# Performance work log

Hardware: AMD Instinct MI355X
Metric: run time of the kernel (lower is better)

## Reference

```python
import jax, jax.numpy as jnp
import numpy as np

B, T, IN, H, FC, OUT = 512, 1024, 64, 128, 128, 1


def _glorot(key, shape, fan):
    bound = 1.0 / np.sqrt(fan)
    return jax.random.uniform(key, shape, jnp.float32, -bound, bound)


def setup_inputs() -> dict:
    key = jax.random.key(0)
    ks = jax.random.split(key, 16)
    inp = {"x": jax.random.normal(ks[0], (B, T, IN), jnp.float32)}
    # GRU layer 0 (input IN -> H), layer 1 (H -> H). PyTorch layout: [3H, in], [3H, H]
    inp["W_ih0"] = _glorot(ks[1], (3 * H, IN), H)
    inp["W_hh0"] = _glorot(ks[2], (3 * H, H), H)
    inp["b_ih0"] = _glorot(ks[3], (3 * H,), H)
    inp["b_hh0"] = _glorot(ks[4], (3 * H,), H)
    inp["W_ih1"] = _glorot(ks[5], (3 * H, H), H)
    inp["W_hh1"] = _glorot(ks[6], (3 * H, H), H)
    inp["b_ih1"] = _glorot(ks[7], (3 * H,), H)
    inp["b_hh1"] = _glorot(ks[8], (3 * H,), H)
    inp["fc1_w"] = _glorot(ks[9], (FC, H), H)
    inp["fc1_b"] = _glorot(ks[10], (FC,), H)
    inp["fc2_w"] = _glorot(ks[11], (OUT, FC), FC)
    inp["fc2_b"] = _glorot(ks[12], (OUT,), FC)
    return inp


def _gru_layer(x_seq, W_ih, W_hh, b_ih, b_hh):
    # x_seq: [T, B, in]. Precompute all input projections in one big GEMM.
    xg = jnp.einsum("tbi,gi->tbg", x_seq, W_ih) + b_ih  # [T, B, 3H]
    h0 = jnp.zeros((x_seq.shape[1], W_hh.shape[1]), x_seq.dtype)

    def step(h, xg_t):
        hg = h @ W_hh.T + b_hh  # [B, 3H]
        xr, xz, xn = jnp.split(xg_t, 3, axis=-1)
        hr, hz, hn = jnp.split(hg, 3, axis=-1)
        r = jax.nn.sigmoid(xr + hr)
        z = jax.nn.sigmoid(xz + hz)
        n = jnp.tanh(xn + r * hn)
        h_new = (1.0 - z) * n + z * h
        return h_new, h_new

    _, hs = jax.lax.scan(step, h0, xg)
    return hs  # [T, B, H]


def reference(x, W_ih0, W_hh0, b_ih0, b_hh0, W_ih1, W_hh1, b_ih1, b_hh1,
              fc1_w, fc1_b, fc2_w, fc2_b):
    xs = jnp.transpose(x, (1, 0, 2))  # [T, B, IN]
    h1 = _gru_layer(xs, W_ih0, W_hh0, b_ih0, b_hh0)  # dropout inactive (eval)
    h2 = _gru_layer(h1, W_ih1, W_hh1, b_ih1, b_hh1)
    last = h2[-1]  # [B, H] == gru_out[:, -1, :]
    y = jax.nn.relu(last @ fc1_w.T + fc1_b)
    return y @ fc2_w.T + fc2_b  # [B, OUT]
```

## Files before the change

### kernel.cpp

```cpp
#include <hip/hip_runtime.h>
#include <hip/hip_fp16.h>
#include <stdint.h>

#define BB   512
#define TT   1024
#define NIN  64
#define HH   128
#define GG   384
#define RPB  2
#define NWG  (BB / RPB)
#define NTHR (2 * GG)

typedef _Float16 half2v __attribute__((ext_vector_type(2)));

__device__ __forceinline__ float fdot2(uint32_t a, uint32_t b, float c) {
    return __builtin_amdgcn_fdot2(__builtin_bit_cast(half2v, a),
                                  __builtin_bit_cast(half2v, b), c, false);
}
__device__ __forceinline__ uint32_t pack2(float a, float b) {
    half2v v; v[0] = (_Float16)a; v[1] = (_Float16)b;
    return __builtin_bit_cast(uint32_t, v);
}
__device__ __forceinline__ uint4 pack8(const float* p) {
    uint4 r;
    r.x = pack2(p[0], p[1]); r.y = pack2(p[2], p[3]);
    r.z = pack2(p[4], p[5]); r.w = pack2(p[6], p[7]);
    return r;
}
__device__ __forceinline__ float sigm(float xv)     { return 1.f / (1.f + __expf(-xv)); }
__device__ __forceinline__ float tanhfast(float xv) { return 2.f / (1.f + __expf(-2.f * xv)) - 1.f; }

#define R8(M)  M(0) M(1) M(2) M(3) M(4) M(5) M(6) M(7)
#define R16(M) M(0) M(1) M(2) M(3) M(4) M(5) M(6) M(7) \
               M(8) M(9) M(10) M(11) M(12) M(13) M(14) M(15)
#define D4(A_, W_, S_) A_ = fdot2(W_.x, S_.x, A_); A_ = fdot2(W_.y, S_.y, A_); \
                       A_ = fdot2(W_.z, S_.z, A_); A_ = fdot2(W_.w, S_.w, A_);

__global__ __launch_bounds__(NTHR, 3) void gru_fused(
    const float* __restrict__ x,
    const float* __restrict__ Wih0, const float* __restrict__ Whh0,
    const float* __restrict__ bih0, const float* __restrict__ bhh0,
    const float* __restrict__ Wih1, const float* __restrict__ Whh1,
    const float* __restrict__ bih1, const float* __restrict__ bhh1,
    const float* __restrict__ fc1w, const float* __restrict__ fc1b,
    const float* __restrict__ fc2w, const float* __restrict__ fc2b,
    float* __restrict__ out)
{
    __shared__ __align__(16) uint32_t xh[RPB][NIN / 2];
    __shared__ __align__(16) uint32_t h0h[RPB][HH / 2];
    __shared__ __align__(16) uint32_t h1h[RPB][HH / 2];
    __shared__ float h0f[RPB][HH];
    __shared__ float h1f[RPB][HH];
    __shared__ float pX0[RPB][GG], pH0[RPB][GG];
    __shared__ float pX1[RPB][GG], pH1[RPB][GG];

    const int lid  = threadIdx.x;
    const int row0 = blockIdx.x * RPB;
    const bool is0 = (lid < GG);

#define DECLW(i) uint4 A##i; uint4 B##i;
    R16(DECLW)
    float bx, bh;

    if (is0) {
        const int g = lid;
        const float* wh = Whh0 + g * HH;
        const float* wi = Wih0 + g * NIN;
#define LA0(i) A##i = pack8(wh + 8 * (i));
#define LB0(i) B##i = pack8(wi + 8 * (i));
        R16(LA0)
        R8(LB0)
        bx = bih0[g]; bh = bhh0[g];
    } else {
        const int g = lid - GG;
        const float* wh = Whh1 + g * HH;
        const float* wi = Wih1 + g * HH;
        R16(LA0)
        R16(LB0)
        bx = bih1[g]; bh = bhh1[g];
    }

    if (lid < 2 * HH) {
        int r = lid >> 7, j = lid & (HH - 1);
        h0f[r][j] = 0.f; h1f[r][j] = 0.f;
    } else if (lid < 2 * HH + 2 * (HH / 2)) {
        int k2 = lid - 2 * HH;
        int r = k2 >> 6, c = k2 & 63;
        h0h[r][c] = 0u; h1h[r][c] = 0u;
    }

    float xreg = 0.f;
    if (lid >= GG + 2 * HH) {
        int j2 = lid - (GG + 2 * HH);
        int r = j2 >> 6, k = j2 & 63;
        const float* xp = x + (size_t)(row0 + r) * TT * NIN + k;
        ((__half*)&xh[r][0])[k] = __float2half(xp[0]);
        xreg = xp[NIN];
    }
    __syncthreads();

    const uint4* xh0v  = (const uint4*)&xh[0][0];
    const uint4* xh1v  = (const uint4*)&xh[1][0];
    const uint4* h0h0v = (const uint4*)&h0h[0][0];
    const uint4* h0h1v = (const uint4*)&h0h[1][0];
    const uint4* h1h0v = (const uint4*)&h1h[0][0];
    const uint4* h1h1v = (const uint4*)&h1h[1][0];

    for (int i = 0; i <= TT; ++i) {
        if (is0) {
            if (i < TT) {
                float ax0 = bx, ax1 = bx, ah0 = bh, ah1 = bh;
#define DX0(i) { uint4 s0 = xh0v[i], s1 = xh1v[i]; D4(ax0, B##i, s0) D4(ax1, B##i, s1) }
                R8(DX0)
#define DH0(i) { uint4 s0 = h0h0v[i], s1 = h0h1v[i]; D4(ah0, A##i, s0) D4(ah1, A##i, s1) }
                R16(DH0)
                pX0[0][lid] = ax0; pX0[1][lid] = ax1;
                pH0[0][lid] = ah0; pH0[1][lid] = ah1;
            }
        } else {
            if (i >= 1) {
                const int g = lid - GG;
                float ax0 = bx, ax1 = bx, ah0 = bh, ah1 = bh;
#define DL1(i) { uint4 p0 = h0h0v[i], p1 = h0h1v[i], q0 = h1h0v[i], q1 = h1h1v[i]; \
                 D4(ax0, B##i, p0) D4(ax1, B##i, p1) D4(ah0, A##i, q0) D4(ah1, A##i, q1) }
                R16(DL1)
                pX1[0][g] = ax0; pX1[1][g] = ax1;
                pH1[0][g] = ah0; pH1[1][g] = ah1;
            }
        }
        __syncthreads();

        if (lid < 2 * HH) {
            if (i < TT) {
                int r = lid >> 7, j = lid & (HH - 1);
                float sr = pX0[r][j]          + pH0[r][j];
                float sz = pX0[r][HH + j]     + pH0[r][HH + j];
                float xn = pX0[r][2 * HH + j];
                float hn = pH0[r][2 * HH + j];
                float rg = sigm(sr);
                float zg = sigm(sz);
                float ng = tanhfast(fmaf(rg, hn, xn));
                float hnew = fmaf(zg, h0f[r][j] - ng, ng);
                h0f[r][j] = hnew;
                ((__half*)&h0h[r][0])[j] = __float2half(hnew);
            }
        } else if (lid >= GG && lid < GG + 2 * HH) {
            if (i >= 1) {
                int t2 = lid - GG;
                int r = t2 >> 7, j = t2 & (HH - 1);
                float sr = pX1[r][j]          + pH1[r][j];
                float sz = pX1[r][HH + j]     + pH1[r][HH + j];
                float xn = pX1[r][2 * HH + j];
                float hn = pH1[r][2 * HH + j];
                float rg = sigm(sr);
                float zg = sigm(sz);
                float ng = tanhfast(fmaf(rg, hn, xn));
                float hnew = fmaf(zg, h1f[r][j] - ng, ng);
                h1f[r][j] = hnew;
                ((__half*)&h1h[r][0])[j] = __float2half(hnew);
            }
        } else if (lid >= GG + 2 * HH) {
            int j2 = lid - (GG + 2 * HH);
            int r = j2 >> 6, k = j2 & 63;
            if (i + 1 < TT) ((__half*)&xh[r][0])[k] = __float2half(xreg);
            if (i + 2 < TT) {
                const float* xp = x + (size_t)(row0 + r) * TT * NIN + (size_t)(i + 2) * NIN + k;
                xreg = xp[0];
            }
        }
        __syncthreads();
    }

    float yv = 0.f;
    if (lid < 2 * HH) {
        int r = lid >> 7, j = lid & (HH - 1);
        const float* fr = fc1w + j * HH;
        float acc = fc1b[j];
        #pragma unroll 8
        for (int k = 0; k < HH; ++k) acc = fmaf(fr[k], h1f[r][k], acc);
        yv = fmaxf(acc, 0.f) * fc2w[j];
        #pragma unroll
        for (int m = 1; m < 64; m <<= 1) yv += __shfl_xor(yv, m, 64);
    }
    __syncthreads();
    if (lid < 2 * HH && (lid & 63) == 0) pX0[0][lid >> 6] = yv;
    __syncthreads();
    if (lid < RPB) out[row0 + lid] = pX0[0][2 * lid] + pX0[0][2 * lid + 1] + fc2b[0];
}

extern "C" void kernel_launch(void* const* d_in, const int* in_sizes, int n_in,
                              void* d_out, int out_size, void* d_ws, size_t ws_size,
                              hipStream_t stream) {
    const float* x    = (const float*)d_in[0];
    const float* Wih0 = (const float*)d_in[1];
    const float* Whh0 = (const float*)d_in[2];
    const float* bih0 = (const float*)d_in[3];
    const float* bhh0 = (const float*)d_in[4];
    const float* Wih1 = (const float*)d_in[5];
    const float* Whh1 = (const float*)d_in[6];
    const float* bih1 = (const float*)d_in[7];
    const float* bhh1 = (const float*)d_in[8];
    const float* fc1w = (const float*)d_in[9];
    const float* fc1b = (const float*)d_in[10];
    const float* fc2w = (const float*)d_in[11];
    const float* fc2b = (const float*)d_in[12];

    gru_fused<<<dim3(NWG), dim3(NTHR), 0, stream>>>(
        x, Wih0, Whh0, bih0, bhh0, Wih1, Whh1, bih1, bhh1,
        fc1w, fc1b, fc2w, fc2b, (float*)d_out);
}
```

Baseline: 2.216 ms.

## Repartition GRU matvec work across thread groups with split-K and multi-gate outputs

Reassigns the 768 threads so each computes several gate outputs (3 or 4) over half the reduction dimension, rather than one gate output over the full dimension. Partial sums go to double-width shared buffers and are added in the gate-update phase. Shared-memory reads of the hidden state now feed more FMAs each, and the layer-1 input and recurrent projections run on separate thread groups. The x staging buffer is double-buffered and loaded as float2. The cost is extra shared-memory partial-sum traffic and additions, plus possible divergence across the more finely split roles.

```diff
diff --git a/kernel.cpp b/kernel.cpp
--- a/kernel.cpp
+++ b/kernel.cpp
@@ -2,14 +2,14 @@
 #include <hip/hip_fp16.h>
 #include <stdint.h>
 
-#define BB   512
 #define TT   1024
 #define NIN  64
 #define HH   128
 #define GG   384
 #define RPB  2
-#define NWG  (BB / RPB)
-#define NTHR (2 * GG)
+#define NWG  256
+#define NTHR 768
+
 
 typedef _Float16 half2v __attribute__((ext_vector_type(2)));
 
@@ -17,24 +17,29 @@
     return __builtin_amdgcn_fdot2(__builtin_bit_cast(half2v, a),
                                   __builtin_bit_cast(half2v, b), c, false);
 }
-__device__ __forceinline__ uint32_t pack2(float a, float b) {
+__device__ __forceinline__ uint32_t pack2f(float a, float b) {
     half2v v; v[0] = (_Float16)a; v[1] = (_Float16)b;
     return __builtin_bit_cast(uint32_t, v);
 }
 __device__ __forceinline__ uint4 pack8(const float* p) {
     uint4 r;
-    r.x = pack2(p[0], p[1]); r.y = pack2(p[2], p[3]);
-    r.z = pack2(p[4], p[5]); r.w = pack2(p[6], p[7]);
+    r.x = pack2f(p[0], p[1]); r.y = pack2f(p[2], p[3]);
+    r.z = pack2f(p[4], p[5]); r.w = pack2f(p[6], p[7]);
     return r;
 }
-__device__ __forceinline__ float sigm(float xv)     { return 1.f / (1.f + __expf(-xv)); }
-__device__ __forceinline__ float tanhfast(float xv) { return 2.f / (1.f + __expf(-2.f * xv)) - 1.f; }
-
-#define R8(M)  M(0) M(1) M(2) M(3) M(4) M(5) M(6) M(7)
-#define R16(M) M(0) M(1) M(2) M(3) M(4) M(5) M(6) M(7) \
-               M(8) M(9) M(10) M(11) M(12) M(13) M(14) M(15)
+__device__ __forceinline__ float sigm(float v)     { return 1.f / (1.f + __expf(-v)); }
+__device__ __forceinline__ float tanhfast(float v) { return 2.f / (1.f + __expf(-2.f * v)) - 1.f; }
+
 #define D4(A_, W_, S_) A_ = fdot2(W_.x, S_.x, A_); A_ = fdot2(W_.y, S_.y, A_); \
                        A_ = fdot2(W_.z, S_.z, A_); A_ = fdot2(W_.w, S_.w, A_);
+
+#define PK8(M_, g_) M_(g_,0) M_(g_,1) M_(g_,2) M_(g_,3) M_(g_,4) M_(g_,5) M_(g_,6) M_(g_,7)
+#define R8X(M_)     M_(0) M_(1) M_(2) M_(3) M_(4) M_(5) M_(6) M_(7)
+#define DWDEF(g_,k_) uint4 W##g_##_##k_;
+#define LW(g_,k_)    W##g_##_##k_ = pack8(wp + (g_)*ws + (k_)*8);
+#define DG(g_,k_) D4(a##g_##_0, W##g_##_##k_, s0_) D4(a##g_##_1, W##g_##_##k_, s1_)
+#define SK4(k_) { uint4 s0_ = pb0[k_], s1_ = pb1[k_]; DG(0,k_) DG(1,k_) DG(2,k_) DG(3,k_) }
+#define SK3(k_) { uint4 s0_ = pb0[k_], s1_ = pb1[k_]; DG(0,k_) DG(1,k_) DG(2,k_) }
 
 __global__ __launch_bounds__(NTHR, 3) void gru_fused(
     const float* __restrict__ x,
@@ -46,134 +51,155 @@
     const float* __restrict__ fc2w, const float* __restrict__ fc2b,
     float* __restrict__ out)
 {
-    __shared__ __align__(16) uint32_t xh[RPB][NIN / 2];
+    __shared__ __align__(16) uint32_t xh[2][RPB][NIN / 2];
     __shared__ __align__(16) uint32_t h0h[RPB][HH / 2];
     __shared__ __align__(16) uint32_t h1h[RPB][HH / 2];
     __shared__ float h0f[RPB][HH];
     __shared__ float h1f[RPB][HH];
-    __shared__ float pX0[RPB][GG], pH0[RPB][GG];
-    __shared__ float pX1[RPB][GG], pH1[RPB][GG];
+    __shared__ float pX0[RPB][GG];
+    __shared__ float pH0h[2][RPB][GG];
+    __shared__ float pX1h[2][RPB][GG];
+    __shared__ float pH1h[2][RPB][GG];
 
     const int lid  = threadIdx.x;
     const int row0 = blockIdx.x * RPB;
-    const bool is0 = (lid < GG);
-
-#define DECLW(i) uint4 A##i; uint4 B##i;
-    R16(DECLW)
-    float bx, bh;
-
-    if (is0) {
-        const int g = lid;
-        const float* wh = Whh0 + g * HH;
-        const float* wi = Wih0 + g * NIN;
-#define LA0(i) A##i = pack8(wh + 8 * (i));
-#define LB0(i) B##i = pack8(wi + 8 * (i));
-        R16(LA0)
-        R8(LB0)
-        bx = bih0[g]; bh = bhh0[g];
+
+    PK8(DWDEF,0) PK8(DWDEF,1) PK8(DWDEF,2) PK8(DWDEF,3)
+    float b0 = 0.f, b1 = 0.f, b2 = 0.f, b3 = 0.f;
+    int gq_ = 0, kh_ = 0;
+    const uint4 *pbA0 = nullptr, *pbA1 = nullptr;
+    float2 xr2 = {0.f, 0.f};
+
+    if (lid < 128) {
+        const int t = lid;
+        const float* wp = Wih0 + (3 * t) * NIN; const int ws = NIN;
+        PK8(LW,0) PK8(LW,1) PK8(LW,2)
+        b0 = bih0[3 * t]; b1 = bih0[3 * t + 1]; b2 = bih0[3 * t + 2];
+    } else if (lid < 320) {
+        const int t = lid - 128; gq_ = t >> 1; kh_ = t & 1;
+        const float* wp = Whh0 + (4 * gq_) * HH + kh_ * 64; const int ws = HH;
+        PK8(LW,0) PK8(LW,1) PK8(LW,2) PK8(LW,3)
+        if (!kh_) { b0 = bhh0[4*gq_]; b1 = bhh0[4*gq_+1]; b2 = bhh0[4*gq_+2]; b3 = bhh0[4*gq_+3]; }
+        pbA0 = (const uint4*)&h0h[0][0] + kh_ * 8;
+        pbA1 = (const uint4*)&h0h[1][0] + kh_ * 8;
+    } else if (lid < 512) {
+        const int t = lid - 320; gq_ = t >> 1; kh_ = t & 1;
+        const float* wp = Wih1 + (4 * gq_) * HH + kh_ * 64; const int ws = HH;
+        PK8(LW,0) PK8(LW,1) PK8(LW,2) PK8(LW,3)
+        if (!kh_) { b0 = bih1[4*gq_]; b1 = bih1[4*gq_+1]; b2 = bih1[4*gq_+2]; b3 = bih1[4*gq_+3]; }
+        pbA0 = (const uint4*)&h0h[0][0] + kh_ * 8;
+        pbA1 = (const uint4*)&h0h[1][0] + kh_ * 8;
+    } else if (lid < 704) {
+        const int t = lid - 512; gq_ = t >> 1; kh_ = t & 1;
+        const float* wp = Whh1 + (4 * gq_) * HH + kh_ * 64; const int ws = HH;
+        PK8(LW,0) PK8(LW,1) PK8(LW,2) PK8(LW,3)
+        if (!kh_) { b0 = bhh1[4*gq_]; b1 = bhh1[4*gq_+1]; b2 = bhh1[4*gq_+2]; b3 = bhh1[4*gq_+3]; }
+        pbA0 = (const uint4*)&h1h[0][0] + kh_ * 8;
+        pbA1 = (const uint4*)&h1h[1][0] + kh_ * 8;
     } else {
-        const int g = lid - GG;
-        const float* wh = Whh1 + g * HH;
-        const float* wi = Wih1 + g * HH;
-        R16(LA0)
-        R16(LB0)
-        bx = bih1[g]; bh = bhh1[g];
-    }
-
-    if (lid < 2 * HH) {
-        int r = lid >> 7, j = lid & (HH - 1);
+        const int idx = lid - 704, r = idx >> 5, c = idx & 31;
+        const float* xp = x + (size_t)(row0 + r) * TT * NIN + 2 * c;
+        xh[0][r][c] = pack2f(xp[0], xp[1]);
+        xr2 = *(const float2*)(xp + NIN);
+    }
+
+    if (lid < 128) {
+        int r = lid >> 6, c = lid & 63;
+        h0h[r][c] = 0u; h1h[r][c] = 0u;
+    }
+    if (lid < 256) {
+        int r = lid >> 7, j = lid & 127;
         h0f[r][j] = 0.f; h1f[r][j] = 0.f;
-    } else if (lid < 2 * HH + 2 * (HH / 2)) {
-        int k2 = lid - 2 * HH;
-        int r = k2 >> 6, c = k2 & 63;
-        h0h[r][c] = 0u; h1h[r][c] = 0u;
-    }
-
-    float xreg = 0.f;
-    if (lid >= GG + 2 * HH) {
-        int j2 = lid - (GG + 2 * HH);
-        int r = j2 >> 6, k = j2 & 63;
-        const float* xp = x + (size_t)(row0 + r) * TT * NIN + k;
-        ((__half*)&xh[r][0])[k] = __float2half(xp[0]);
-        xreg = xp[NIN];
     }
     __syncthreads();
 
-    const uint4* xh0v  = (const uint4*)&xh[0][0];
-    const uint4* xh1v  = (const uint4*)&xh[1][0];
-    const uint4* h0h0v = (const uint4*)&h0h[0][0];
-    const uint4* h0h1v = (const uint4*)&h0h[1][0];
-    const uint4* h1h0v = (const uint4*)&h1h[0][0];
-    const uint4* h1h1v = (const uint4*)&h1h[1][0];
-
     for (int i = 0; i <= TT; ++i) {
-        if (is0) {
+        if (lid < 128) {
             if (i < TT) {
-                float ax0 = bx, ax1 = bx, ah0 = bh, ah1 = bh;
-#define DX0(i) { uint4 s0 = xh0v[i], s1 = xh1v[i]; D4(ax0, B##i, s0) D4(ax1, B##i, s1) }
-                R8(DX0)
-#define DH0(i) { uint4 s0 = h0h0v[i], s1 = h0h1v[i]; D4(ah0, A##i, s0) D4(ah1, A##i, s1) }
-                R16(DH0)
-                pX0[0][lid] = ax0; pX0[1][lid] = ax1;
-                pH0[0][lid] = ah0; pH0[1][lid] = ah1;
+                const uint4* pb0 = (const uint4*)&xh[i & 1][0][0];
+                const uint4* pb1 = (const uint4*)&xh[i & 1][1][0];
+                float a0_0 = b0, a0_1 = b0, a1_0 = b1, a1_1 = b1, a2_0 = b2, a2_1 = b2;
+                R8X(SK3)
+                const int g0 = 3 * lid;
+                pX0[0][g0] = a0_0; pX0[0][g0+1] = a1_0; pX0[0][g0+2] = a2_0;
+                pX0[1][g0] = a0_1; pX0[1][g0+1] = a1_1; pX0[1][g0+2] = a2_1;
+            }
+        } else if (lid < 320) {
+            if (i < TT) {
+                const uint4 *pb0 = pbA0, *pb1 = pbA1;
+                float a0_0=b0,a0_1=b0,a1_0=b1,a1_1=b1,a2_0=b2,a2_1=b2,a3_0=b3,a3_1=b3;
+                R8X(SK4)
+                float4 v0 = {a0_0, a1_0, a2_0, a3_0};
+                float4 v1 = {a0_1, a1_1, a2_1, a3_1};
+                *(float4*)&pH0h[kh_][0][4 * gq_] = v0;
+                *(float4*)&pH0h[kh_][1][4 * gq_] = v1;
+            }
+        } else if (lid < 512) {
+            if (i >= 1) {
+                const uint4 *pb0 = pbA0, *pb1 = pbA1;
+                float a0_0=b0,a0_1=b0,a1_0=b1,a1_1=b1,a2_0=b2,a2_1=b2,a3_0=b3,a3_1=b3;
+                R8X(SK4)
+                float4 v0 = {a0_0, a1_0, a2_0, a3_0};
+                float4 v1 = {a0_1, a1_1, a2_1, a3_1};
+                *(float4*)&pX1h[kh_][0][4 * gq_] = v0;
+                *(float4*)&pX1h[kh_][1][4 * gq_] = v1;
+            }
+        } else if (lid < 704) {
+            if (i >= 1) {
+                const uint4 *pb0 = pbA0, *pb1 = pbA1;
+                float a0_0=b0,a0_1=b0,a1_0=b1,a1_1=b1,a2_0=b2,a2_1=b2,a3_0=b3,a3_1=b3;
+                R8X(SK4)
+                float4 v0 = {a0_0, a1_0, a2_0, a3_0};
+                float4 v1 = {a0_1, a1_1, a2_1, a3_1};
+                *(float4*)&pH1h[kh_][0][4 * gq_] = v0;
+                *(float4*)&pH1h[kh_][1][4 * gq_] = v1;
             }
         } else {
-            if (i >= 1) {
-                const int g = lid - GG;
-                float ax0 = bx, ax1 = bx, ah0 = bh, ah1 = bh;
-#define DL1(i) { uint4 p0 = h0h0v[i], p1 = h0h1v[i], q0 = h1h0v[i], q1 = h1h1v[i]; \
-                 D4(ax0, B##i, p0) D4(ax1, B##i, p1) D4(ah0, A##i, q0) D4(ah1, A##i, q1) }
-                R16(DL1)
-                pX1[0][g] = ax0; pX1[1][g] = ax1;
-                pH1[0][g] = ah0; pH1[1][g] = ah1;
-            }
+            const int idx = lid - 704, r = idx >> 5, c = idx & 31;
+            if (i + 1 < TT) xh[(i + 1) & 1][r][c] = pack2f(xr2.x, xr2.y);
+            if (i + 2 < TT)
+                xr2 = *(const float2*)(x + (size_t)(row0 + r) * TT * NIN
+                                         + (size_t)(i + 2) * NIN + 2 * c);
         }
         __syncthreads();
 
-        if (lid < 2 * HH) {
+        if (lid < 256) {
             if (i < TT) {
-                int r = lid >> 7, j = lid & (HH - 1);
-                float sr = pX0[r][j]          + pH0[r][j];
-                float sz = pX0[r][HH + j]     + pH0[r][HH + j];
-                float xn = pX0[r][2 * HH + j];
-                float hn = pH0[r][2 * HH + j];
-                float rg = sigm(sr);
-                float zg = sigm(sz);
-                float ng = tanhfast(fmaf(rg, hn, xn));
+                const int r = lid >> 7, j = lid & 127;
+                float xr_ = pX0[r][j], xz_ = pX0[r][HH + j], xn_ = pX0[r][2*HH + j];
+                float hr_ = pH0h[0][r][j]        + pH0h[1][r][j];
+                float hz_ = pH0h[0][r][HH + j]   + pH0h[1][r][HH + j];
+                float hn_ = pH0h[0][r][2*HH + j] + pH0h[1][r][2*HH + j];
+                float rg = sigm(xr_ + hr_);
+                float zg = sigm(xz_ + hz_);
+                float ng = tanhfast(fmaf(rg, hn_, xn_));
                 float hnew = fmaf(zg, h0f[r][j] - ng, ng);
                 h0f[r][j] = hnew;
                 ((__half*)&h0h[r][0])[j] = __float2half(hnew);
             }
-        } else if (lid >= GG && lid < GG + 2 * HH) {
+        } else if (lid < 512) {
             if (i >= 1) {
-                int t2 = lid - GG;
-                int r = t2 >> 7, j = t2 & (HH - 1);
-                float sr = pX1[r][j]          + pH1[r][j];
-                float sz = pX1[r][HH + j]     + pH1[r][HH + j];
-                float xn = pX1[r][2 * HH + j];
-                float hn = pH1[r][2 * HH + j];
-                float rg = sigm(sr);
-                float zg = sigm(sz);
-                float ng = tanhfast(fmaf(rg, hn, xn));
+                const int t = lid - 256, r = t >> 7, j = t & 127;
+                float xr_ = pX1h[0][r][j]        + pX1h[1][r][j];
+                float xz_ = pX1h[0][r][HH + j]   + pX1h[1][r][HH + j];
+                float xn_ = pX1h[0][r][2*HH + j] + pX1h[1][r][2*HH + j];
+                float hr_ = pH1h[0][r][j]        + pH1h[1][r][j];
+                float hz_ = pH1h[0][r][HH + j]   + pH1h[1][r][HH + j];
+                float hn_ = pH1h[0][r][2*HH + j] + pH1h[1][r][2*HH + j];
+                float rg = sigm(xr_ + hr_);
+                float zg = sigm(xz_ + hz_);
+                float ng = tanhfast(fmaf(rg, hn_, xn_));
                 float hnew = fmaf(zg, h1f[r][j] - ng, ng);
                 h1f[r][j] = hnew;
                 ((__half*)&h1h[r][0])[j] = __float2half(hnew);
             }
-        } else if (lid >= GG + 2 * HH) {
-            int j2 = lid - (GG + 2 * HH);
-            int r = j2 >> 6, k = j2 & 63;
-            if (i + 1 < TT) ((__half*)&xh[r][0])[k] = __float2half(xreg);
-            if (i + 2 < TT) {
-                const float* xp = x + (size_t)(row0 + r) * TT * NIN + (size_t)(i + 2) * NIN + k;
-                xreg = xp[0];
-            }
         }
         __syncthreads();
     }
 
     float yv = 0.f;
-    if (lid < 2 * HH) {
-        int r = lid >> 7, j = lid & (HH - 1);
+    if (lid < 256) {
+        const int r = lid >> 7, j = lid & 127;
         const float* fr = fc1w + j * HH;
         float acc = fc1b[j];
         #pragma unroll 8
@@ -183,7 +209,7 @@
         for (int m = 1; m < 64; m <<= 1) yv += __shfl_xor(yv, m, 64);
     }
     __syncthreads();
-    if (lid < 2 * HH && (lid & 63) == 0) pX0[0][lid >> 6] = yv;
+    if (lid < 256 && (lid & 63) == 0) pX0[0][lid >> 6] = yv;
     __syncthreads();
     if (lid < RPB) out[row0 + lid] = pX0[0][2 * lid] + pX0[0][2 * lid + 1] + fc2b[0];
 }
```

Result: faster. 2.140 ms (-3.4%).
